# Optimization experiments

Measured on AMD Instinct MI355X. Metric: run time of the kernel, lower is better.

The kernel has to match this reference:

```python
import jax, jax.numpy as jnp
import numpy as np

B, C, H, W = 8, 128, 128, 128
PLANES, K, STRIDE, PAD = 128, 3, 1, 1
BN_EPS = 1e-5


def setup_inputs() -> dict:
    key = jax.random.key(0)
    k1, k2, k3, k4 = jax.random.split(key, 4)
    x = jax.random.normal(k1, (B, C, H, W), jnp.float32)
    # ConvOffset2D: Conv2d(C, 2C, 3, pad=1, bias=False), weights ~ N(0, 0.01)
    w_off = jax.random.normal(k2, (2 * C, C, 3, 3), jnp.float32) * 0.01
    w_conv = jax.random.normal(k3, (PLANES, C, K, K), jnp.float32) * 0.05
    b_conv = jax.random.normal(k4, (PLANES,), jnp.float32) * 0.01
    gamma = jnp.ones((PLANES,), jnp.float32)
    beta = jnp.zeros((PLANES,), jnp.float32)
    return {"x": x, "w_off": w_off, "w_conv": w_conv, "b_conv": b_conv,
            "gamma": gamma, "beta": beta}


def _conv2d(x, w, stride, pad):
    return jax.lax.conv_general_dilated(
        x, w, window_strides=(stride, stride),
        padding=[(pad, pad), (pad, pad)],
        dimension_numbers=("NCHW", "OIHW", "NCHW"))


def _deform_sample(x, offsets):
    """x: (B,C,H,W); offsets: (B,2C,H,W) -> bilinear offset-sampled (B,C,H,W).
    Faithful to ConvOffset2D: raw reshape (b,2c,h,w) -> (b*c, h*w, 2),
    coords = offsets + meshgrid(i,j), clamp, bilinear interp."""
    b, c, h, w = x.shape
    off = offsets.reshape(b * c, h * w, 2)              # quirky but faithful reshape
    grid = jnp.stack(jnp.meshgrid(jnp.arange(h, dtype=x.dtype),
                                  jnp.arange(w, dtype=x.dtype),
                                  indexing="ij"), axis=-1).reshape(1, h * w, 2)
    coords = off + grid                                  # (b*c, h*w, 2)
    yc = jnp.clip(coords[..., 0], 0.0, h - 1.0)
    xc = jnp.clip(coords[..., 1], 0.0, w - 1.0)
    y0, y1 = jnp.floor(yc), jnp.ceil(yc)
    x0, x1 = jnp.floor(xc), jnp.ceil(xc)
    img = x.reshape(b * c, h * w)

    def gather(yy, xx):
        idx = (yy * w + xx).astype(jnp.int32)
        return jnp.take_along_axis(img, idx, axis=1)

    v_lt = gather(y0, x0)
    v_rb = gather(y1, x1)
    v_lb = gather(y0, x1)
    v_rt = gather(y1, x0)
    dy = yc - y0
    dx = xc - x0
    v_t = v_lt + (v_rt - v_lt) * dy   # interp along height
    v_b = v_lb + (v_rb - v_lb) * dy
    out = v_t + (v_b - v_t) * dx      # interp along width
    return out.reshape(b, c, h, w)


def reference(x, w_off, w_conv, b_conv, gamma, beta):
    offsets = _conv2d(x, w_off, 1, 1)                    # (B, 2C, H, W)
    x_off = _deform_sample(x, offsets)                   # (B, C, H, W)
    y = _conv2d(x_off, w_conv, STRIDE, PAD) + b_conv[None, :, None, None]
    y = jax.nn.relu(y)
    # BatchNorm2d in training mode: batch statistics, biased variance
    mean = y.mean(axis=(0, 2, 3), keepdims=True)
    var = jnp.square(y - mean).mean(axis=(0, 2, 3), keepdims=True)
    y = (y - mean) * jax.lax.rsqrt(var + BN_EPS)
    return y * gamma[None, :, None, None] + beta[None, :, None, None]
```

## Files before the change

kernel.cpp:

```cpp
#include <hip/hip_runtime.h>

#define B_   8
#define C_   128
#define H_   128
#define W_   128
#define HW_  16384

typedef short v8s __attribute__((ext_vector_type(8)));
typedef float v4f __attribute__((ext_vector_type(4)));

#define ROWB 4160

__device__ __forceinline__ float bf2f(unsigned short u) {
  unsigned int v = ((unsigned int)u) << 16;
  float f; __builtin_memcpy(&f, &v, 4); return f;
}
__device__ __forceinline__ unsigned short f2us(float f) {
  unsigned int u; __builtin_memcpy(&u, &f, 4);
  u += 0x7fffu + ((u >> 16) & 1u);
  return (unsigned short)(u >> 16);
}

__global__ __launch_bounds__(256) void prep(const float* __restrict__ x,
                                            unsigned short* __restrict__ xt,
                                            const float* __restrict__ w_off,
                                            const float* __restrict__ w_conv,
                                            unsigned short* __restrict__ pack_off,
                                            unsigned short* __restrict__ pack_main,
                                            uint4* __restrict__ zb) {
  __shared__ alignas(16) unsigned short t[32 * 132];
  const int bid = blockIdx.x, tid = threadIdx.x;
  if (bid < 4096) {
    const int j0 = (bid & 3) * 32, i = (bid >> 2) & 127, b = bid >> 9;
    for (int e = tid; e < 1024; e += 256) {
      int c = e >> 3, j4 = (e & 7) << 2;
      float4 v = *(const float4*)&x[((b * C_ + c) * H_ + i) * W_ + j0 + j4];
      t[(j4 + 0) * 132 + c] = f2us(v.x);
      t[(j4 + 1) * 132 + c] = f2us(v.y);
      t[(j4 + 2) * 132 + c] = f2us(v.z);
      t[(j4 + 3) * 132 + c] = f2us(v.w);
    }
    __syncthreads();
    for (int f = tid; f < 1024; f += 256) {
      int cg = f >> 7, g = f & 127;
      int j = g >> 2, c4 = (g & 3) << 2;
      uint2 v = *(const uint2*)&t[j * 132 + cg * 16 + c4];
      *(uint2*)(xt + ((size_t)(b * 8 + cg) * HW_ + i * W_ + j0 + j) * 16 + c4) = v;
    }
    return;
  }
  const int pb = bid - 4096;
  if (pb == 0) zb[tid] = (uint4){0u, 0u, 0u, 0u};
  const float* w;
  unsigned short* pack;
  int G, idx;
  if (pb < 1280) { w = w_off;  pack = pack_off;  G = 16; idx = pb * 256 + tid; }
  else           { w = w_conv; pack = pack_main; G = 8;  idx = (pb - 1280) * 256 + tid; }
  if (idx >= 20480 * G) return;
  int j  = idx & 7;
  int l  = (idx >> 3) & 63;
  int g  = (idx >> 9) % G;
  int t2 = idx / (512 * G);
  int pp = t2 % 5;
  int cc = t2 / 5;
  int oc = g * 16 + (l & 15);
  int kk = ((l >> 4) << 3) + j;
  int ic = (cc << 4) + (kk & 15);
  int rs = pp * 2 + (kk >> 4);
  float v = (rs < 9) ? w[(oc * C_ + ic) * 9 + rs] : 0.f;
  pack[idx] = f2us(v);
}

template <int MODE, int G>
__global__ __launch_bounds__(512, 4) void conv_gemm(const unsigned short* __restrict__ xt,
                                                    const unsigned short* __restrict__ pack,
                                                    const float* __restrict__ bias,
                                                    const char* __restrict__ zb,
                                                    unsigned short* __restrict__ outp,
                                                    float* __restrict__ ps) {
  __shared__ alignas(16) char rawb[4 * ROWB];
  __shared__ float bs1[128], bs2[128];

  const int nb = blockIdx.x;
  int b, ip, mt;
  {
    int xcd = nb & 7, r = nb >> 3;
    if (MODE == 0) { b = r >> 4; mt = (r >> 3) & 1; ip = xcd * 8 + (r & 7); }
    else           { b = r >> 3; mt = 0;            ip = xcd * 8 + (r & 7); }
  }
  const int i0 = ip * 2;
  const int tid  = threadIdx.x;
  const int lane = tid & 63, wid = tid >> 6;
  const int q = lane >> 4, n = lane & 15;
  const int wr = wid & 1, wm = (wid >> 1) & 1, wn = wid >> 2;

  if (MODE == 1 && tid < 128) { bs1[tid] = 0.f; bs2[tid] = 0.f; }
  if (tid < 16) {
    int r = tid >> 2, rem = tid & 3, side = rem >> 1, h = rem & 1;
    *(uint4*)(rawb + r * ROWB + (side ? 129 * 32 : 0) + h * 16) = (uint4){0u,0u,0u,0u};
  }

  int boff[5];
#pragma unroll
  for (int pp = 0; pp < 5; ++pp) {
    int rs = pp * 2 + (q >> 1);
    if (rs > 8) rs = 8;
    int dr = (rs >= 6) ? 2 : ((rs >= 3) ? 1 : 0);
    int s = rs - dr * 3;
    boff[pp] = (wr + dr) * ROWB + s * 32 + (q & 1) * 16;
  }
  const int pcol = (wn * 64 + n) * 32;

  v4f acc[4][4];
#pragma unroll
  for (int a = 0; a < 4; ++a)
#pragma unroll
    for (int c = 0; c < 4; ++c) acc[a][c] = (v4f){0.f, 0.f, 0.f, 0.f};

  const v8s* packv = (const v8s*)pack;
  const int gbase = mt * 8 + wm * 4;

  for (int cc = 0; cc < 8; ++cc) {
    __syncthreads();
    const char* ccbase = (const char*)xt + (size_t)(b * 8 + cc) * (HW_ * 32);
#pragma unroll
    for (int t = 0; t < 2; ++t) {
      int c = wid * 2 + t, r = c >> 2, k = c & 3;
      int ii = i0 + r - 1;
      const char* src = ((unsigned)ii < 128u)
                          ? ccbase + ii * 4096 + k * 1024 + lane * 16
                          : zb + lane * 16;
      __builtin_amdgcn_global_load_lds(
          (const __attribute__((address_space(1))) unsigned int*)src,
          (__attribute__((address_space(3))) unsigned int*)(rawb + r * ROWB + 32 + k * 1024),
          16, 0, 0);
    }
    __syncthreads();

#pragma unroll
    for (int pp = 0; pp < 5; ++pp) {
      const v8s* ap = packv + ((cc * 5 + pp) * G + gbase) * 64 + lane;
      v8s Af[4];
#pragma unroll
      for (int fm = 0; fm < 4; ++fm) Af[fm] = ap[fm * 64];
      v8s Bf[4];
#pragma unroll
      for (int fn = 0; fn < 4; ++fn)
        Bf[fn] = *(const v8s*)(rawb + boff[pp] + pcol + fn * 512);
#pragma unroll
      for (int fm = 0; fm < 4; ++fm) {
#pragma unroll
        for (int fn = 0; fn < 4; ++fn)
          acc[fm][fn] = __builtin_amdgcn_mfma_f32_16x16x32_bf16(Af[fm], Bf[fn],
                                                                acc[fm][fn], 0, 0, 0);
      }
    }
  }

  const int OC = G * 16;
  const int ob = (b * OC + mt * 128 + wm * 64) * HW_ + (i0 + wr) * W_ + wn * 64;

  if (MODE == 0) {
#pragma unroll
    for (int fm = 0; fm < 4; ++fm)
#pragma unroll
      for (int fn = 0; fn < 4; ++fn)
#pragma unroll
        for (int rr = 0; rr < 4; ++rr)
          outp[ob + (fm * 16 + q * 4 + rr) * HW_ + fn * 16 + n] = f2us(acc[fm][fn][rr]);
  } else {
    float bv[4][4], s1a[4][4], s2a[4][4];
#pragma unroll
    for (int fm = 0; fm < 4; ++fm)
#pragma unroll
      for (int rr = 0; rr < 4; ++rr) {
        bv[fm][rr] = bias[wm * 64 + fm * 16 + q * 4 + rr];
        s1a[fm][rr] = 0.f; s2a[fm][rr] = 0.f;
      }
#pragma unroll
    for (int fm = 0; fm < 4; ++fm)
#pragma unroll
      for (int fn = 0; fn < 4; ++fn)
#pragma unroll
        for (int rr = 0; rr < 4; ++rr) {
          float v = acc[fm][fn][rr] + bv[fm][rr];
          v = fmaxf(v, 0.f);
          outp[ob + (fm * 16 + q * 4 + rr) * HW_ + fn * 16 + n] = f2us(v);
          s1a[fm][rr] += v; s2a[fm][rr] += v * v;
        }
#pragma unroll
    for (int fm = 0; fm < 4; ++fm)
#pragma unroll
      for (int rr = 0; rr < 4; ++rr) {
        float s1 = s1a[fm][rr], s2 = s2a[fm][rr];
#pragma unroll
        for (int m = 1; m < 16; m <<= 1) {
          s1 += __shfl_xor(s1, m);
          s2 += __shfl_xor(s2, m);
        }
        if (n == 0) {
          atomicAdd(&bs1[wm * 64 + fm * 16 + q * 4 + rr], s1);
          atomicAdd(&bs2[wm * 64 + fm * 16 + q * 4 + rr], s2);
        }
      }
    __syncthreads();
    if (tid < 128) {
      ps[nb * 128 + tid]          = bs1[tid];
      ps[131072 + nb * 128 + tid] = bs2[tid];
    }
  }
}

__global__ __launch_bounds__(256) void deform_t(const float* __restrict__ x,
                                                const unsigned short* __restrict__ offs,
                                                unsigned short* __restrict__ xofft) {
  const int gid = blockIdx.x * 256 + threadIdx.x;
  const int pix = gid & (HW_ - 1);
  const int bcg = gid >> 14;
  const int b = bcg >> 3, cg = bcg & 7;
  const int i = pix >> 7, j = pix & 127;
  const float fi = (float)i, fj = (float)j;
  const float* xb = x + (((size_t)b * C_) << 14);
  const unsigned short* ob = offs + ((size_t)b << 22) + 2 * (size_t)pix;
  unsigned int packed[8];
#pragma unroll
  for (int u = 0; u < 16; ++u) {
    const int c = cg * 16 + u;
    unsigned int pr = *(const unsigned int*)(ob + ((size_t)c << 15));
    float oy = bf2f((unsigned short)(pr & 0xffffu));
    float ox = bf2f((unsigned short)(pr >> 16));
    float yc = fminf(fmaxf(oy + fi, 0.f), 127.f);
    float xc = fminf(fmaxf(ox + fj, 0.f), 127.f);
    float y0f = floorf(yc), y1f = ceilf(yc);
    float x0f = floorf(xc), x1f = ceilf(xc);
    int y0 = (int)y0f, y1 = (int)y1f, x0 = (int)x0f, x1 = (int)x1f;
    const float* img = xb + (c << 14);
    float v_lt = img[y0 * W_ + x0];
    float v_rb = img[y1 * W_ + x1];
    float v_lb = img[y0 * W_ + x1];
    float v_rt = img[y1 * W_ + x0];
    float dy = yc - y0f, dx = xc - x0f;
    float v_t = v_lt + (v_rt - v_lt) * dy;
    float v_b = v_lb + (v_rb - v_lb) * dy;
    float o   = v_t + (v_b - v_t) * dx;
    unsigned int us = (unsigned int)f2us(o);
    if (u & 1) packed[u >> 1] |= us << 16;
    else       packed[u >> 1]  = us;
  }
  uint4* dst = (uint4*)(xofft + ((size_t)gid << 4));
  dst[0] = (uint4){packed[0], packed[1], packed[2], packed[3]};
  dst[1] = (uint4){packed[4], packed[5], packed[6], packed[7]};
}

__global__ __launch_bounds__(256) void bn_finalize(const float* __restrict__ ps,
                                                   const float* __restrict__ gamma,
                                                   const float* __restrict__ beta,
                                                   float* __restrict__ stats) {
  const int c = blockIdx.x, tid = threadIdx.x;
  float s1 = 0.f, s2 = 0.f;
  for (int k = tid; k < 512; k += 256) {
    s1 += ps[k * 128 + c];
    s2 += ps[131072 + k * 128 + c];
  }
#pragma unroll
  for (int m = 32; m > 0; m >>= 1) {
    s1 += __shfl_down(s1, m);
    s2 += __shfl_down(s2, m);
  }
  __shared__ float l1[4], l2[4];
  int wid = tid >> 6;
  if ((tid & 63) == 0) { l1[wid] = s1; l2[wid] = s2; }
  __syncthreads();
  if (tid == 0) {
    s1 = l1[0] + l1[1] + l1[2] + l1[3];
    s2 = l2[0] + l2[1] + l2[2] + l2[3];
    const float invn = 1.f / 131072.f;
    float mean = s1 * invn;
    float var  = s2 * invn - mean * mean;
    float inv  = rsqrtf(var + 1e-5f);
    float sc = gamma[c] * inv;
    stats[c]       = sc;
    stats[128 + c] = beta[c] - mean * sc;
  }
}

__global__ __launch_bounds__(256) void bn_apply(const unsigned short* __restrict__ y,
                                                const float* __restrict__ stats,
                                                float* __restrict__ out) {
  int gid = blockIdx.x * 256 + threadIdx.x;
  int base = gid << 4;
  int c = (base >> 14) & 127;
  float sc = stats[c], sh = stats[128 + c];
  uint4 u0 = ((const uint4*)y)[gid * 2];
  uint4 u1 = ((const uint4*)y)[gid * 2 + 1];
  const unsigned short* us0 = (const unsigned short*)&u0;
  const unsigned short* us1 = (const unsigned short*)&u1;
  float4 o[4];
#pragma unroll
  for (int k = 0; k < 4; ++k) {
    const unsigned short* s = (k < 2) ? us0 + k * 4 : us1 + (k - 2) * 4;
    o[k].x = bf2f(s[0]) * sc + sh;
    o[k].y = bf2f(s[1]) * sc + sh;
    o[k].z = bf2f(s[2]) * sc + sh;
    o[k].w = bf2f(s[3]) * sc + sh;
  }
#pragma unroll
  for (int k = 0; k < 4; ++k) ((float4*)out)[gid * 4 + k] = o[k];
}

extern "C" void kernel_launch(void* const* d_in, const int* in_sizes, int n_in,
                              void* d_out, int out_size, void* d_ws, size_t ws_size,
                              hipStream_t stream) {
  const float* x      = (const float*)d_in[0];
  const float* w_off  = (const float*)d_in[1];
  const float* w_conv = (const float*)d_in[2];
  const float* b_conv = (const float*)d_in[3];
  const float* gamma  = (const float*)d_in[4];
  const float* beta   = (const float*)d_in[5];
  float* out = (float*)d_out;

  char* ws = (char*)d_ws;
  unsigned short* x_t    = (unsigned short*)ws;
  unsigned short* xoff_t = (unsigned short*)ws;
  unsigned short* offs = (unsigned short*)(ws + 33554432);
  unsigned short* yws  = (unsigned short*)(ws + 33554432);
  float* ps    = (float*)(ws + 67108864);
  float* stats = (float*)(ws + 68157440);
  unsigned short* pack_off  = (unsigned short*)(ws + 100663296);
  unsigned short* pack_main = (unsigned short*)(ws + 101318656);
  char* zb = ws + 101646336;

  prep<<<6016, 256, 0, stream>>>(x, x_t, w_off, w_conv, pack_off, pack_main,
                                 (uint4*)zb);
  conv_gemm<0, 16><<<1024, 512, 0, stream>>>(x_t, pack_off, nullptr, zb, offs, nullptr);
  deform_t<<<4096, 256, 0, stream>>>(x, offs, xoff_t);
  conv_gemm<1, 8><<<512, 512, 0, stream>>>(xoff_t, pack_main, b_conv, zb, yws, ps);
  bn_finalize<<<128, 256, 0, stream>>>(ps, gamma, beta, stats);
  bn_apply<<<4096, 256, 0, stream>>>(yws, stats, out);
}
```

Baseline: 304.9 us.

## Fuse deformable bilinear sampling into offset-conv GEMM epilogue via shared memory

The offset convolution GEMM now stages its bf16 offset tile in shared memory and performs the bilinear deformable sampling directly in its epilogue, writing the transposed sampled tensor. The separate deform kernel and the global round trip of the offsets tensor are removed. This relies on the quirky reshape mapping letting each block own the offset channels it needs (two rows i and i+64). Shared memory for MODE 0 grows to about 66KB, which reduces occupancy relative to the declared launch bounds.

```diff
diff --git a/kernel.cpp b/kernel.cpp
--- a/kernel.cpp
+++ b/kernel.cpp
@@ -76,9 +76,10 @@
                                                     const unsigned short* __restrict__ pack,
                                                     const float* __restrict__ bias,
                                                     const char* __restrict__ zb,
+                                                    const float* __restrict__ x,
                                                     unsigned short* __restrict__ outp,
                                                     float* __restrict__ ps) {
-  __shared__ alignas(16) char rawb[4 * ROWB];
+  __shared__ alignas(16) char rawb[MODE == 0 ? 67584 : 16640];
   __shared__ float bs1[128], bs2[128];
 
   const int nb = blockIdx.x;
@@ -157,18 +158,61 @@
     }
   }
 
-  const int OC = G * 16;
-  const int ob = (b * OC + mt * 128 + wm * 64) * HW_ + (i0 + wr) * W_ + wn * 64;
-
   if (MODE == 0) {
+    unsigned short* ot = (unsigned short*)rawb;
+    __syncthreads();
 #pragma unroll
     for (int fm = 0; fm < 4; ++fm)
 #pragma unroll
       for (int fn = 0; fn < 4; ++fn)
 #pragma unroll
-        for (int rr = 0; rr < 4; ++rr)
-          outp[ob + (fm * 16 + q * 4 + rr) * HW_ + fn * 16 + n] = f2us(acc[fm][fn][rr]);
+        for (int rr = 0; rr < 4; ++rr) {
+          int oc_l = wm * 64 + fm * 16 + q * 4 + rr;
+          int col  = wn * 64 + fn * 16 + n;
+          ot[oc_l * 264 + wr * 132 + col] = f2us(acc[fm][fn][rr]);
+        }
+    __syncthreads();
+    const float* xb = x + (((size_t)b * C_) << 14);
+    for (int s = tid; s < 1024; s += 512) {
+      int px = s & 127, isel = (s >> 7) & 1, cgl = s >> 8;
+      int di = ip + isel * 64;
+      const float fi = (float)di, fj = (float)px;
+      int cy = 2 * px, cx = 2 * px + 1;
+      int ry = cy >> 7, coly = cy & 127;
+      int rx = cx >> 7, colx = cx & 127;
+      unsigned int packed[8];
+#pragma unroll
+      for (int u = 0; u < 16; ++u) {
+        int c_l = cgl * 16 + u;
+        int chl = 2 * c_l + isel;
+        float oy = bf2f(ot[chl * 264 + ry * 132 + coly]);
+        float ox = bf2f(ot[chl * 264 + rx * 132 + colx]);
+        float yc = fminf(fmaxf(oy + fi, 0.f), 127.f);
+        float xc = fminf(fmaxf(ox + fj, 0.f), 127.f);
+        float y0f = floorf(yc), y1f = ceilf(yc);
+        float x0f = floorf(xc), x1f = ceilf(xc);
+        int y0 = (int)y0f, y1 = (int)y1f, x0 = (int)x0f, x1 = (int)x1f;
+        const float* img = xb + ((mt * 64 + c_l) << 14);
+        float v_lt = img[y0 * W_ + x0];
+        float v_rb = img[y1 * W_ + x1];
+        float v_lb = img[y0 * W_ + x1];
+        float v_rt = img[y1 * W_ + x0];
+        float dy = yc - y0f, dx = xc - x0f;
+        float v_t = v_lt + (v_rt - v_lt) * dy;
+        float v_b = v_lb + (v_rb - v_lb) * dy;
+        float o   = v_t + (v_b - v_t) * dx;
+        unsigned int us = (unsigned int)f2us(o);
+        if (u & 1) packed[u >> 1] |= us << 16;
+        else       packed[u >> 1]  = us;
+      }
+      unsigned short* dst =
+          outp + ((size_t)((b * 8 + mt * 4 + cgl) * HW_ + di * W_ + px) << 4);
+      ((uint4*)dst)[0] = (uint4){packed[0], packed[1], packed[2], packed[3]};
+      ((uint4*)dst)[1] = (uint4){packed[4], packed[5], packed[6], packed[7]};
+    }
   } else {
+    const int OC = G * 16;
+    const int ob = (b * OC + mt * 128 + wm * 64) * HW_ + (i0 + wr) * W_ + wn * 64;
     float bv[4][4], s1a[4][4], s2a[4][4];
 #pragma unroll
     for (int fm = 0; fm < 4; ++fm)
@@ -209,47 +253,6 @@
       ps[131072 + nb * 128 + tid] = bs2[tid];
     }
   }
-}
-
-__global__ __launch_bounds__(256) void deform_t(const float* __restrict__ x,
-                                                const unsigned short* __restrict__ offs,
-                                                unsigned short* __restrict__ xofft) {
-  const int gid = blockIdx.x * 256 + threadIdx.x;
-  const int pix = gid & (HW_ - 1);
-  const int bcg = gid >> 14;
-  const int b = bcg >> 3, cg = bcg & 7;
-  const int i = pix >> 7, j = pix & 127;
-  const float fi = (float)i, fj = (float)j;
-  const float* xb = x + (((size_t)b * C_) << 14);
-  const unsigned short* ob = offs + ((size_t)b << 22) + 2 * (size_t)pix;
-  unsigned int packed[8];
-#pragma unroll
-  for (int u = 0; u < 16; ++u) {
-    const int c = cg * 16 + u;
-    unsigned int pr = *(const unsigned int*)(ob + ((size_t)c << 15));
-    float oy = bf2f((unsigned short)(pr & 0xffffu));
-    float ox = bf2f((unsigned short)(pr >> 16));
-    float yc = fminf(fmaxf(oy + fi, 0.f), 127.f);
-    float xc = fminf(fmaxf(ox + fj, 0.f), 127.f);
-    float y0f = floorf(yc), y1f = ceilf(yc);
-    float x0f = floorf(xc), x1f = ceilf(xc);
-    int y0 = (int)y0f, y1 = (int)y1f, x0 = (int)x0f, x1 = (int)x1f;
-    const float* img = xb + (c << 14);
-    float v_lt = img[y0 * W_ + x0];
-    float v_rb = img[y1 * W_ + x1];
-    float v_lb = img[y0 * W_ + x1];
-    float v_rt = img[y1 * W_ + x0];
-    float dy = yc - y0f, dx = xc - x0f;
-    float v_t = v_lt + (v_rt - v_lt) * dy;
-    float v_b = v_lb + (v_rb - v_lb) * dy;
-    float o   = v_t + (v_b - v_t) * dx;
-    unsigned int us = (unsigned int)f2us(o);
-    if (u & 1) packed[u >> 1] |= us << 16;
-    else       packed[u >> 1]  = us;
-  }
-  uint4* dst = (uint4*)(xofft + ((size_t)gid << 4));
-  dst[0] = (uint4){packed[0], packed[1], packed[2], packed[3]};
-  dst[1] = (uint4){packed[4], packed[5], packed[6], packed[7]};
 }
 
 __global__ __launch_bounds__(256) void bn_finalize(const float* __restrict__ ps,
@@ -321,9 +324,8 @@
 
   char* ws = (char*)d_ws;
   unsigned short* x_t    = (unsigned short*)ws;
-  unsigned short* xoff_t = (unsigned short*)ws;
-  unsigned short* offs = (unsigned short*)(ws + 33554432);
-  unsigned short* yws  = (unsigned short*)(ws + 33554432);
+  unsigned short* xoff_t = (unsigned short*)(ws + 33554432);
+  unsigned short* yws    = (unsigned short*)ws;
   float* ps    = (float*)(ws + 67108864);
   float* stats = (float*)(ws + 68157440);
   unsigned short* pack_off  = (unsigned short*)(ws + 100663296);
@@ -332,9 +334,10 @@
 
   prep<<<6016, 256, 0, stream>>>(x, x_t, w_off, w_conv, pack_off, pack_main,
                                  (uint4*)zb);
-  conv_gemm<0, 16><<<1024, 512, 0, stream>>>(x_t, pack_off, nullptr, zb, offs, nullptr);
-  deform_t<<<4096, 256, 0, stream>>>(x, offs, xoff_t);
-  conv_gemm<1, 8><<<512, 512, 0, stream>>>(xoff_t, pack_main, b_conv, zb, yws, ps);
+  conv_gemm<0, 16><<<1024, 512, 0, stream>>>(x_t, pack_off, nullptr, zb, x,
+                                             xoff_t, nullptr);
+  conv_gemm<1, 8><<<512, 512, 0, stream>>>(xoff_t, pack_main, b_conv, zb, nullptr,
+                                           yws, ps);
   bn_finalize<<<128, 256, 0, stream>>>(ps, gamma, beta, stats);
   bn_apply<<<4096, 256, 0, stream>>>(yws, stats, out);
 }
```

After: 309.7 us. About the same (+1.6%).
